# Performance work log

Hardware: AMD Instinct MI355X
Metric: run time of the kernel (lower is better)

## Reference

```python
import jax, jax.numpy as jnp
import numpy as np

B, C, H, W = 32, 64, 32, 32
DIM = H * W          # number of tokens (pixels)
DEPTH = 8
TAU = 1.0
NUM_CLASSES = 10


def setup_inputs() -> dict:
    key = jax.random.key(0)
    ks = jax.random.split(key, 6)
    return {
        "image": jax.random.normal(ks[0], (B, C, H, W), dtype=jnp.float32),
        "WV": 10.0 * jax.random.normal(ks[1], (C, C), dtype=jnp.float32),
        "WK": jax.random.normal(ks[2], (C, C), dtype=jnp.float32),
        "WQ": jax.random.normal(ks[3], (C, C), dtype=jnp.float32),
        "last_W": jax.random.normal(ks[4], (NUM_CLASSES, DIM), dtype=jnp.float32) / np.sqrt(DIM),
        "last_b": jnp.zeros((NUM_CLASSES,), dtype=jnp.float32),
    }


def reference(image, WV, WK, WQ, last_W, last_b):
    # flatten(2).transpose(1,2): (B,C,H,W) -> (B, H*W, C)
    X = image.reshape(B, C, DIM).transpose(0, 2, 1)
    scale = DIM ** (-0.5)
    for _ in range(DEPTH):
        # weight_sharing=True, sign=0 -> W = WV every layer
        Q = X @ WQ                                  # (B, n, C)
        K = X @ WK                                  # (B, n, C)
        scores = jnp.einsum('bnc,bmc->bnm', Q, K) * scale  # (B, n, n)
        A = jax.nn.softmax(scores, axis=-1)
        # diffusion_step (method 'A'): tau * A @ (X @ W) + X
        X = TAU * jnp.einsum('bnm,bmc->bnc', A, X @ WV) + X
    # mean over channel dim -> (B, dim), then Linear(dim, num_classes)
    pred = X.mean(-1) @ last_W.T + last_b
    return pred
```

## Files before the change

### kernel.cpp

```cpp
#include <hip/hip_runtime.h>
#include <math.h>

#define BB    32
#define CCH   64
#define DIMN  1024
#define NCLS  10

typedef __attribute__((ext_vector_type(8))) short bf16x8;
typedef __attribute__((ext_vector_type(4))) float f32x4;
typedef __attribute__((ext_vector_type(4))) unsigned short us4;
typedef __attribute__((ext_vector_type(8))) unsigned short us8;

#define MFMA16(a, b, c) __builtin_amdgcn_mfma_f32_16x16x32_bf16(a, b, c, 0, 0, 0)

__device__ __forceinline__ unsigned short f2bf(float x) {
  unsigned u = __float_as_uint(x);
  unsigned r = u + 0x7fffu + ((u >> 16) & 1u);
  return (unsigned short)(r >> 16);
}
__device__ __forceinline__ float bf2f(unsigned short h) {
  return __uint_as_float(((unsigned)h) << 16);
}
__device__ __forceinline__ void split3_pk(float x0, float x1,
                                          unsigned& hp, unsigned& mp,
                                          unsigned& lp) {
  unsigned h, m, l;
  asm("v_cvt_pk_bf16_f32 %0, %1, %2" : "=v"(h) : "v"(x0), "v"(x1));
  const float h0 = __uint_as_float(h << 16);
  const float h1 = __uint_as_float(h & 0xffff0000u);
  const float r0 = x0 - h0, r1 = x1 - h1;
  asm("v_cvt_pk_bf16_f32 %0, %1, %2" : "=v"(m) : "v"(r0), "v"(r1));
  const float m0 = __uint_as_float(m << 16);
  const float m1 = __uint_as_float(m & 0xffff0000u);
  asm("v_cvt_pk_bf16_f32 %0, %1, %2" : "=v"(l) : "v"(r0 - m0), "v"(r1 - m1));
  hp = h; mp = m; lp = l;
}
__device__ __forceinline__ void split3_pk2(float x0, float x1,
    unsigned short& h0, unsigned short& m0, unsigned short& l0,
    unsigned short& h1, unsigned short& m1, unsigned short& l1) {
  unsigned h, m, l;
  split3_pk(x0, x1, h, m, l);
  h0 = (unsigned short)h; h1 = (unsigned short)(h >> 16);
  m0 = (unsigned short)m; m1 = (unsigned short)(m >> 16);
  l0 = (unsigned short)l; l1 = (unsigned short)(l >> 16);
}
__device__ __forceinline__ void split3_frag(const float* xv, bf16x8& fh,
                                            bf16x8& fm, bf16x8& fl) {
  union U { bf16x8 v; unsigned d[4]; } uh, um, ul;
  #pragma unroll
  for (int p = 0; p < 4; ++p)
    split3_pk(xv[2 * p], xv[2 * p + 1], uh.d[p], um.d[p], ul.d[p]);
  fh = uh.v; fm = um.v; fl = ul.v;
}
__device__ __forceinline__ bf16x8 ld16B(const unsigned short* p) {
  union { us8 u; bf16x8 v; } c;
  c.u = *(const us8*)p;
  return c.v;
}

__global__ __launch_bounds__(256) void k_transpose(const float* __restrict__ img,
                                                   float* __restrict__ X) {
  __shared__ float tile[64][65];
  const int b  = blockIdx.y;
  const int n0 = blockIdx.x * 64;
  const int tx = threadIdx.x & 63;
  const int ty = threadIdx.x >> 6;
  const float* src = img + (size_t)b * CCH * DIMN;
  #pragma unroll
  for (int c = ty; c < 64; c += 4)
    tile[c][tx] = src[(size_t)c * DIMN + n0 + tx];
  __syncthreads();
  float* dst = X + (size_t)b * DIMN * CCH;
  #pragma unroll
  for (int nn = ty; nn < 64; nn += 4)
    dst[(size_t)(n0 + nn) * CCH + tx] = tile[tx][nn];
}

__global__ __launch_bounds__(256) void k_qkv_split(
    const float* __restrict__ X,
    const float* __restrict__ WQ, const float* __restrict__ WK,
    const float* __restrict__ WV,
    float* __restrict__ Q,
    unsigned short* __restrict__ Kh, unsigned short* __restrict__ Km,
    unsigned short* __restrict__ Kl,
    unsigned short* __restrict__ VhT, unsigned short* __restrict__ VmT,
    unsigned short* __restrict__ VlT) {
  __shared__ float xs[16][64];
  __shared__ unsigned short vs[3][16][64];
  const int c  = threadIdx.x & 63;
  const int tg = threadIdx.x >> 6;
  const size_t t0 = (size_t)blockIdx.x * 16;
  #pragma unroll
  for (int r = tg; r < 16; r += 4)
    xs[r][c] = X[(t0 + r) * 64 + c];
  __syncthreads();
  float qa[4] = {0.f,0.f,0.f,0.f};
  float ka[4] = {0.f,0.f,0.f,0.f};
  float va[4] = {0.f,0.f,0.f,0.f};
  for (int j = 0; j < 64; ++j) {
    const float wq = WQ[j * 64 + c];
    const float wk = WK[j * 64 + c];
    const float wv = WV[j * 64 + c];
    #pragma unroll
    for (int r = 0; r < 4; ++r) {
      const float x = xs[tg * 4 + r][j];
      qa[r] = fmaf(x, wq, qa[r]);
      ka[r] = fmaf(x, wk, ka[r]);
      va[r] = fmaf(x, wv, va[r]);
    }
  }
  #pragma unroll
  for (int pr = 0; pr < 2; ++pr) {
    const int r0 = 2 * pr, r1 = 2 * pr + 1;
    const int ta = tg * 4 + r0, tb = tg * 4 + r1;
    const size_t ia = (t0 + ta) * 64 + c;
    const size_t ib = (t0 + tb) * 64 + c;
    Q[ia] = qa[r0]; Q[ib] = qa[r1];
    unsigned short h0, m0, l0, h1, m1, l1;
    split3_pk2(ka[r0], ka[r1], h0, m0, l0, h1, m1, l1);
    Kh[ia] = h0; Km[ia] = m0; Kl[ia] = l0;
    Kh[ib] = h1; Km[ib] = m1; Kl[ib] = l1;
    split3_pk2(va[r0], va[r1], h0, m0, l0, h1, m1, l1);
    vs[0][ta][c] = h0; vs[1][ta][c] = m0; vs[2][ta][c] = l0;
    vs[0][tb][c] = h1; vs[1][tb][c] = m1; vs[2][tb][c] = l1;
  }
  __syncthreads();
  {
    const int row  = threadIdx.x >> 2;
    const int part = threadIdx.x & 3;
    const size_t bofs = (t0 >> 10) * ((size_t)DIMN * 64);
    const size_t kt   = (t0 & 1023) >> 5;
    const size_t tin  = (size_t)part * 8 + ((t0 & 31) >> 2);
    unsigned short* dst[3] = {VhT, VmT, VlT};
    #pragma unroll
    for (int term = 0; term < 3; ++term) {
      us4 pk;
      #pragma unroll
      for (int i = 0; i < 4; ++i) pk[i] = vs[term][part * 4 + i][row];
      *(us4*)&dst[term][bofs + kt * 2048 + (size_t)row * 32 + tin] = pk;
    }
  }
}

__global__ __launch_bounds__(256) void k_qkv_merge(
    float* __restrict__ X,
    const float* __restrict__ Mp, const float* __restrict__ Lp,
    const float* __restrict__ Op,
    const float* __restrict__ WQ, const float* __restrict__ WK,
    const float* __restrict__ WV,
    float* __restrict__ Q,
    unsigned short* __restrict__ Kh, unsigned short* __restrict__ Km,
    unsigned short* __restrict__ Kl,
    unsigned short* __restrict__ VhT, unsigned short* __restrict__ VmT,
    unsigned short* __restrict__ VlT) {
  __shared__ float xs[16][64];
  __shared__ unsigned short vs[3][16][64];
  const int c  = threadIdx.x & 63;
  const int tg = threadIdx.x >> 6;
  const size_t t0 = (size_t)blockIdx.x * 16;
  #pragma unroll
  for (int r = tg; r < 16; r += 4) {
    const size_t grow = t0 + r;
    const float m0 = Mp[grow], m1 = Mp[32768 + grow];
    const float l0 = Lp[grow], l1 = Lp[32768 + grow];
    const float mm = fmaxf(m0, m1);
    const float w0 = __expf(m0 - mm), w1 = __expf(m1 - mm);
    const float inv = 1.0f / (l0 * w0 + l1 * w1);
    const float o0 = Op[grow * 64 + c];
    const float o1 = Op[(size_t)2097152 + grow * 64 + c];
    const float xn = X[grow * 64 + c] + (o0 * w0 + o1 * w1) * inv;
    X[grow * 64 + c] = xn;
    xs[r][c] = xn;
  }
  __syncthreads();
  float qa[4] = {0.f,0.f,0.f,0.f};
  float ka[4] = {0.f,0.f,0.f,0.f};
  float va[4] = {0.f,0.f,0.f,0.f};
  for (int j = 0; j < 64; ++j) {
    const float wq = WQ[j * 64 + c];
    const float wk = WK[j * 64 + c];
    const float wv = WV[j * 64 + c];
    #pragma unroll
    for (int r = 0; r < 4; ++r) {
      const float x = xs[tg * 4 + r][j];
      qa[r] = fmaf(x, wq, qa[r]);
      ka[r] = fmaf(x, wk, ka[r]);
      va[r] = fmaf(x, wv, va[r]);
    }
  }
  #pragma unroll
  for (int pr = 0; pr < 2; ++pr) {
    const int r0 = 2 * pr, r1 = 2 * pr + 1;
    const int ta = tg * 4 + r0, tb = tg * 4 + r1;
    const size_t ia = (t0 + ta) * 64 + c;
    const size_t ib = (t0 + tb) * 64 + c;
    Q[ia] = qa[r0]; Q[ib] = qa[r1];
    unsigned short h0, m0, l0, h1, m1, l1;
    split3_pk2(ka[r0], ka[r1], h0, m0, l0, h1, m1, l1);
    Kh[ia] = h0; Km[ia] = m0; Kl[ia] = l0;
    Kh[ib] = h1; Km[ib] = m1; Kl[ib] = l1;
    split3_pk2(va[r0], va[r1], h0, m0, l0, h1, m1, l1);
    vs[0][ta][c] = h0; vs[1][ta][c] = m0; vs[2][ta][c] = l0;
    vs[0][tb][c] = h1; vs[1][tb][c] = m1; vs[2][tb][c] = l1;
  }
  __syncthreads();
  {
    const int row  = threadIdx.x >> 2;
    const int part = threadIdx.x & 3;
    const size_t bofs = (t0 >> 10) * ((size_t)DIMN * 64);
    const size_t kt   = (t0 & 1023) >> 5;
    const size_t tin  = (size_t)part * 8 + ((t0 & 31) >> 2);
    unsigned short* dst[3] = {VhT, VmT, VlT};
    #pragma unroll
    for (int term = 0; term < 3; ++term) {
      us4 pk;
      #pragma unroll
      for (int i = 0; i < 4; ++i) pk[i] = vs[term][part * 4 + i][row];
      *(us4*)&dst[term][bofs + kt * 2048 + (size_t)row * 32 + tin] = pk;
    }
  }
}

__global__ __launch_bounds__(256, 4) void k_attn_sk(
    const float* __restrict__ Qg,
    const unsigned short* __restrict__ Kh, const unsigned short* __restrict__ Km,
    const unsigned short* __restrict__ Kl,
    const unsigned short* __restrict__ VhT, const unsigned short* __restrict__ VmT,
    const unsigned short* __restrict__ VlT,
    float* __restrict__ Mp, float* __restrict__ Lp, float* __restrict__ Op) {
  __shared__ __align__(16) unsigned short Khs[32 * 72];
  __shared__ __align__(16) unsigned short Kms[32 * 72];
  __shared__ __align__(16) unsigned short Kls[32 * 72];
  __shared__ __align__(16) unsigned short Vhs[64 * 40];
  __shared__ __align__(16) unsigned short Vms[64 * 40];
  __shared__ __align__(16) unsigned short Vls[64 * 40];

  const int tid  = threadIdx.x;
  const int w    = tid >> 6;
  const int lane = tid & 63;
  const int ln   = lane & 15;
  const int q    = lane >> 4;

  const int bid   = blockIdx.x;
  const int xcd   = bid & 7;
  const int seq   = bid >> 3;
  const int b     = xcd * 4 + (seq >> 5);
  const int local = seq & 31;
  const int half  = local >> 4;
  const int i0    = (local & 15) * 64;

  const size_t base = (size_t)b * (DIMN * 64);
  const float scale = 0.03125f;

  const int kj = tid >> 3, kg = tid & 7;
  const int vc = tid >> 2, vg = tid & 3;
  const int klo = kj * 72 + kg * 8;
  const int vlo = vc * 40 + vg * 8;

  bf16x8 qh[2], qm[2], ql[2];
  {
    const int mrow = i0 + 16 * w + ln;
    const float* qp = Qg + base + (size_t)mrow * 64 + 8 * q;
    #pragma unroll
    for (int s = 0; s < 2; ++s) {
      const float4 x0 = ((const float4*)(qp + 32 * s))[0];
      const float4 x1 = ((const float4*)(qp + 32 * s))[1];
      const float xv[8] = {x0.x, x0.y, x0.z, x0.w, x1.x, x1.y, x1.z, x1.w};
      split3_frag(xv, qh[s], qm[s], ql[s]);
    }
  }

  f32x4 O[4];
  #pragma unroll
  for (int ct = 0; ct < 4; ++ct) O[ct] = (f32x4){0.f, 0.f, 0.f, 0.f};
  float m_run = -INFINITY;
  float l_run = 0.f;

  const int kt0 = half * 16;
  for (int kt = kt0; kt < kt0 + 16; ++kt) {
    __syncthreads();

    {
      const size_t tof = base + (size_t)kt * 2048 + tid * 8;
      const us8 a0 = *(const us8*)&Kh[tof];
      const us8 a1 = *(const us8*)&Km[tof];
      const us8 a2 = *(const us8*)&Kl[tof];
      const us8 b0 = *(const us8*)&VhT[tof];
      const us8 b1 = *(const us8*)&VmT[tof];
      const us8 b2 = *(const us8*)&VlT[tof];
      *(us8*)&Khs[klo] = a0;
      *(us8*)&Kms[klo] = a1;
      *(us8*)&Kls[klo] = a2;
      *(us8*)&Vhs[vlo] = b0;
      *(us8*)&Vms[vlo] = b1;
      *(us8*)&Vls[vlo] = b2;
    }
    __syncthreads();

    f32x4 sacc[2];
    __builtin_amdgcn_s_setprio(1);
    #pragma unroll
    for (int ct = 0; ct < 2; ++ct) {
      f32x4 a = (f32x4){0.f, 0.f, 0.f, 0.f};
      #pragma unroll
      for (int s = 0; s < 2; ++s) {
        const int ko = (16 * ct + ln) * 72 + 32 * s + 8 * q;
        const bf16x8 bh = ld16B(&Khs[ko]);
        const bf16x8 bm = ld16B(&Kms[ko]);
        const bf16x8 bl = ld16B(&Kls[ko]);
        a = MFMA16(bh, ql[s], a);
        a = MFMA16(bl, qh[s], a);
        a = MFMA16(bm, qm[s], a);
        a = MFMA16(bh, qm[s], a);
        a = MFMA16(bm, qh[s], a);
        a = MFMA16(bh, qh[s], a);
      }
      sacc[ct] = a;
    }
    __builtin_amdgcn_s_setprio(0);

    float m8 = fmaxf(fmaxf(fmaxf(sacc[0][0], sacc[0][1]),
                           fmaxf(sacc[0][2], sacc[0][3])),
                     fmaxf(fmaxf(sacc[1][0], sacc[1][1]),
                           fmaxf(sacc[1][2], sacc[1][3])));
    m8 = fmaxf(m8, __shfl_xor(m8, 16, 64));
    m8 = fmaxf(m8, __shfl_xor(m8, 32, 64));
    const float mnew  = fmaxf(m_run, m8 * scale);
    const float alpha = __expf(m_run - mnew);
    m_run = mnew;

    float pv[8];
    float s8 = 0.f;
    #pragma unroll
    for (int ct = 0; ct < 2; ++ct) {
      #pragma unroll
      for (int r = 0; r < 4; ++r) {
        const float p = __expf(sacc[ct][r] * scale - m_run);
        pv[ct * 4 + r] = p;
        s8 += p;
      }
    }
    float sr = s8 + __shfl_xor(s8, 16, 64);
    sr = sr + __shfl_xor(sr, 32, 64);
    l_run = l_run * alpha + sr;

    const int srcb = (lane & 48) + ((lane & 48) >> 2);
    float arow[4];
    #pragma unroll
    for (int r = 0; r < 4; ++r) arow[r] = __shfl(alpha, srcb + r, 64);
    #pragma unroll
    for (int ct = 0; ct < 4; ++ct) {
      #pragma unroll
      for (int r = 0; r < 4; ++r) O[ct][r] *= arow[r];
    }

    bf16x8 ph, pm, pl;
    split3_frag(pv, ph, pm, pl);

    __builtin_amdgcn_s_setprio(1);
    #pragma unroll
    for (int ct = 0; ct < 4; ++ct) {
      const int vo = (16 * ct + ln) * 40 + 8 * q;
      const bf16x8 vvh = ld16B(&Vhs[vo]);
      const bf16x8 vvm = ld16B(&Vms[vo]);
      const bf16x8 vvl = ld16B(&Vls[vo]);
      O[ct] = MFMA16(ph, vvh, O[ct]);
      O[ct] = MFMA16(ph, vvm, O[ct]);
      O[ct] = MFMA16(pm, vvh, O[ct]);
      O[ct] = MFMA16(pm, vvm, O[ct]);
      O[ct] = MFMA16(ph, vvl, O[ct]);
      O[ct] = MFMA16(pl, vvh, O[ct]);
    }
    __builtin_amdgcn_s_setprio(0);
  }

  const size_t hofs = (size_t)half * (32 * 1024);
  #pragma unroll
  for (int r = 0; r < 4; ++r) {
    const int row = i0 + 16 * w + 4 * q + r;
    const size_t grow = hofs + (size_t)b * DIMN + row;
    #pragma unroll
    for (int ct = 0; ct < 4; ++ct)
      Op[grow * 64 + ln + 16 * ct] = O[ct][r];
  }
  if (q == 0) {
    const size_t tgrow = hofs + (size_t)b * DIMN + i0 + 16 * w + ln;
    Mp[tgrow] = m_run;
    Lp[tgrow] = l_run;
  }
}

__global__ __launch_bounds__(256) void k_merge_mean(
    const float* __restrict__ X,
    const float* __restrict__ Mp, const float* __restrict__ Lp,
    const float* __restrict__ Op, float* __restrict__ meanv) {
  const int c  = threadIdx.x & 63;
  const int tg = threadIdx.x >> 6;
  const size_t t0 = (size_t)blockIdx.x * 128;
  for (int i = tg; i < 128; i += 4) {
    const size_t grow = t0 + i;
    const float m0 = Mp[grow], m1 = Mp[32768 + grow];
    const float l0 = Lp[grow], l1 = Lp[32768 + grow];
    const float mm = fmaxf(m0, m1);
    const float w0 = __expf(m0 - mm), w1 = __expf(m1 - mm);
    const float inv = 1.0f / (l0 * w0 + l1 * w1);
    const float o0 = Op[grow * 64 + c];
    const float o1 = Op[(size_t)2097152 + grow * 64 + c];
    float v = X[grow * 64 + c] + (o0 * w0 + o1 * w1) * inv;
    #pragma unroll
    for (int off = 32; off > 0; off >>= 1)
      v += __shfl_down(v, off, 64);
    if (c == 0) meanv[grow] = v * (1.0f / 64.0f);
  }
}

__global__ __launch_bounds__(256) void k_head2(
    const float* __restrict__ meanv, const float* __restrict__ lW,
    const float* __restrict__ lb, float* __restrict__ out) {
  __shared__ float red[256];
  const int b   = blockIdx.x;
  const int tid = threadIdx.x;
  float acc[NCLS];
  #pragma unroll
  for (int k = 0; k < NCLS; ++k) acc[k] = 0.f;
  for (int n = tid; n < DIMN; n += 256) {
    const float m = meanv[(size_t)b * DIMN + n];
    #pragma unroll
    for (int k = 0; k < NCLS; ++k)
      acc[k] = fmaf(m, lW[k * DIMN + n], acc[k]);
  }
  for (int k = 0; k < NCLS; ++k) {
    red[tid] = acc[k];
    __syncthreads();
    for (int s = 128; s > 0; s >>= 1) {
      if (tid < s) red[tid] += red[tid + s];
      __syncthreads();
    }
    if (tid == 0) out[b * NCLS + k] = red[0] + lb[k];
    __syncthreads();
  }
}

__global__ __launch_bounds__(256) void k_attn_s(
    const float* __restrict__ Qg,
    const unsigned short* __restrict__ Kh, const unsigned short* __restrict__ Km,
    const unsigned short* __restrict__ Kl,
    const unsigned short* __restrict__ VhT, const unsigned short* __restrict__ VmT,
    const unsigned short* __restrict__ VlT,
    float* __restrict__ X, float* __restrict__ meanout) {
  __shared__ __align__(16) unsigned short Khs[32 * 72];
  __shared__ __align__(16) unsigned short Kms[32 * 72];
  __shared__ __align__(16) unsigned short Kls[32 * 72];
  __shared__ __align__(16) unsigned short Vhs[64 * 40];
  __shared__ __align__(16) unsigned short Vms[64 * 40];
  __shared__ __align__(16) unsigned short Vls[64 * 40];

  const int tid  = threadIdx.x;
  const int w    = tid >> 6;
  const int lane = tid & 63;
  const int ln   = lane & 15;
  const int q    = lane >> 4;
  const int bid = blockIdx.x;
  const int xcd = bid & 7;
  const int seq = bid >> 3;
  const int b   = xcd * 4 + (seq >> 4);
  const int i0  = (seq & 15) * 64;
  const size_t base = (size_t)b * (DIMN * 64);
  const float scale = 0.03125f;

  const int kj = tid >> 3, kg = tid & 7;
  const int vc = tid >> 2, vg = tid & 3;
  const int klo = kj * 72 + kg * 8;
  const int vlo = vc * 40 + vg * 8;

  bf16x8 qh[2], qm[2], ql[2];
  {
    const int mrow = i0 + 16 * w + ln;
    const float* qp = Qg + base + (size_t)mrow * 64 + 8 * q;
    #pragma unroll
    for (int s = 0; s < 2; ++s) {
      const float4 x0 = ((const float4*)(qp + 32 * s))[0];
      const float4 x1 = ((const float4*)(qp + 32 * s))[1];
      const float xv[8] = {x0.x, x0.y, x0.z, x0.w, x1.x, x1.y, x1.z, x1.w};
      split3_frag(xv, qh[s], qm[s], ql[s]);
    }
  }

  f32x4 O[4];
  #pragma unroll
  for (int ct = 0; ct < 4; ++ct) O[ct] = (f32x4){0.f, 0.f, 0.f, 0.f};
  float m_run = -INFINITY;
  float l_run = 0.f;

  for (int kt = 0; kt < 32; ++kt) {
    __syncthreads();
    {
      const size_t tof = base + (size_t)kt * 2048 + tid * 8;
      const us8 a0 = *(const us8*)&Kh[tof];
      const us8 a1 = *(const us8*)&Km[tof];
      const us8 a2 = *(const us8*)&Kl[tof];
      const us8 b0 = *(const us8*)&VhT[tof];
      const us8 b1 = *(const us8*)&VmT[tof];
      const us8 b2 = *(const us8*)&VlT[tof];
      *(us8*)&Khs[klo] = a0;
      *(us8*)&Kms[klo] = a1;
      *(us8*)&Kls[klo] = a2;
      *(us8*)&Vhs[vlo] = b0;
      *(us8*)&Vms[vlo] = b1;
      *(us8*)&Vls[vlo] = b2;
    }
    __syncthreads();

    f32x4 sacc[2];
    __builtin_amdgcn_s_setprio(1);
    #pragma unroll
    for (int ct = 0; ct < 2; ++ct) {
      f32x4 a = (f32x4){0.f, 0.f, 0.f, 0.f};
      #pragma unroll
      for (int s = 0; s < 2; ++s) {
        const int ko = (16 * ct + ln) * 72 + 32 * s + 8 * q;
        const bf16x8 bh = ld16B(&Khs[ko]);
        const bf16x8 bm = ld16B(&Kms[ko]);
        const bf16x8 bl = ld16B(&Kls[ko]);
        a = MFMA16(bh, ql[s], a);
        a = MFMA16(bl, qh[s], a);
        a = MFMA16(bm, qm[s], a);
        a = MFMA16(bh, qm[s], a);
        a = MFMA16(bm, qh[s], a);
        a = MFMA16(bh, qh[s], a);
      }
      sacc[ct] = a;
    }
    __builtin_amdgcn_s_setprio(0);

    float m8 = fmaxf(fmaxf(fmaxf(sacc[0][0], sacc[0][1]),
                           fmaxf(sacc[0][2], sacc[0][3])),
                     fmaxf(fmaxf(sacc[1][0], sacc[1][1]),
                           fmaxf(sacc[1][2], sacc[1][3])));
    m8 = fmaxf(m8, __shfl_xor(m8, 16, 64));
    m8 = fmaxf(m8, __shfl_xor(m8, 32, 64));
    const float mnew  = fmaxf(m_run, m8 * scale);
    const float alpha = __expf(m_run - mnew);
    m_run = mnew;

    float pv[8];
    float s8 = 0.f;
    #pragma unroll
    for (int ct = 0; ct < 2; ++ct) {
      #pragma unroll
      for (int r = 0; r < 4; ++r) {
        const float p = __expf(sacc[ct][r] * scale - m_run);
        pv[ct * 4 + r] = p;
        s8 += p;
      }
    }
    float sr = s8 + __shfl_xor(s8, 16, 64);
    sr = sr + __shfl_xor(sr, 32, 64);
    l_run = l_run * alpha + sr;

    const int srcb = (lane & 48) + ((lane & 48) >> 2);
    float arow[4];
    #pragma unroll
    for (int r = 0; r < 4; ++r) arow[r] = __shfl(alpha, srcb + r, 64);
    #pragma unroll
    for (int ct = 0; ct < 4; ++ct) {
      #pragma unroll
      for (int r = 0; r < 4; ++r) O[ct][r] *= arow[r];
    }

    bf16x8 ph, pm, pl;
    split3_frag(pv, ph, pm, pl);

    __builtin_amdgcn_s_setprio(1);
    #pragma unroll
    for (int ct = 0; ct < 4; ++ct) {
      const int vo = (16 * ct + ln) * 40 + 8 * q;
      const bf16x8 vvh = ld16B(&Vhs[vo]);
      const bf16x8 vvm = ld16B(&Vms[vo]);
      const bf16x8 vvl = ld16B(&Vls[vo]);
      O[ct] = MFMA16(ph, vvh, O[ct]);
      O[ct] = MFMA16(ph, vvm, O[ct]);
      O[ct] = MFMA16(pm, vvh, O[ct]);
      O[ct] = MFMA16(pm, vvm, O[ct]);
      O[ct] = MFMA16(ph, vvl, O[ct]);
      O[ct] = MFMA16(pl, vvh, O[ct]);
    }
    __builtin_amdgcn_s_setprio(0);
  }

  const int srcb = (lane & 48) + ((lane & 48) >> 2);
  float linv[4];
  #pragma unroll
  for (int r = 0; r < 4; ++r) linv[r] = 1.0f / __shfl(l_run, srcb + r, 64);
  #pragma unroll
  for (int r = 0; r < 4; ++r) {
    const int row = i0 + 16 * w + 4 * q + r;
    float srow = 0.f;
    #pragma unroll
    for (int ct = 0; ct < 4; ++ct) {
      float* xp = X + base + (size_t)row * 64 + ln + 16 * ct;
      const float nv = *xp + O[ct][r] * linv[r];
      *xp = nv;
      srow += nv;
    }
    if (meanout) {
      #pragma unroll
      for (int mk = 1; mk <= 8; mk <<= 1)
        srow += __shfl_xor(srow, mk, 64);
      if (ln == 0) meanout[(size_t)b * DIMN + row] = srow * (1.0f / 64.0f);
    }
  }
}

extern "C" void kernel_launch(void* const* d_in, const int* in_sizes, int n_in,
                              void* d_out, int out_size, void* d_ws, size_t ws_size,
                              hipStream_t stream) {
  const float* image = (const float*)d_in[0];
  const float* WV    = (const float*)d_in[1];
  const float* WK    = (const float*)d_in[2];
  const float* WQ    = (const float*)d_in[3];
  const float* lW    = (const float*)d_in[4];
  const float* lb    = (const float*)d_in[5];
  float* out = (float*)d_out;

  float* ws = (float*)d_ws;
  const size_t NELEM = (size_t)BB * DIMN * CCH;
  const size_t NROW  = (size_t)BB * DIMN;

  const size_t need_sk   = (7 * NELEM + 5 * NROW) * sizeof(float);
  const size_t need_fast = (5 * NELEM + NROW) * sizeof(float);

  if (ws_size >= need_sk) {
    float* X = ws;
    float* Q = ws + NELEM;
    unsigned short* Kh  = (unsigned short*)(ws + 2 * NELEM);
    unsigned short* Km  = Kh + NELEM;
    unsigned short* Kl  = Kh + 2 * NELEM;
    unsigned short* VhT = Kh + 3 * NELEM;
    unsigned short* VmT = Kh + 4 * NELEM;
    unsigned short* VlT = Kh + 5 * NELEM;
    float* Op    = ws + 5 * NELEM;
    float* Mp    = ws + 7 * NELEM;
    float* Lp    = Mp + 2 * NROW;
    float* meanv = Lp + 2 * NROW;

    k_transpose<<<dim3(DIMN / 64, BB), 256, 0, stream>>>(image, X);
    k_qkv_split<<<(BB * DIMN) / 16, 256, 0, stream>>>(
        X, WQ, WK, WV, Q, Kh, Km, Kl, VhT, VmT, VlT);
    for (int layer = 0; layer < 8; ++layer) {
      k_attn_sk<<<1024, 256, 0, stream>>>(
          Q, Kh, Km, Kl, VhT, VmT, VlT, Mp, Lp, Op);
      if (layer < 7)
        k_qkv_merge<<<(BB * DIMN) / 16, 256, 0, stream>>>(
            X, Mp, Lp, Op, WQ, WK, WV, Q, Kh, Km, Kl, VhT, VmT, VlT);
    }
    k_merge_mean<<<256, 256, 0, stream>>>(X, Mp, Lp, Op, meanv);
    k_head2<<<BB, 256, 0, stream>>>(meanv, lW, lb, out);
  } else {
    float* X = ws;
    float* Q = ws + NELEM;
    unsigned short* Kh  = (unsigned short*)(ws + 2 * NELEM);
    unsigned short* Km  = Kh + NELEM;
    unsigned short* Kl  = Kh + 2 * NELEM;
    unsigned short* VhT = Kh + 3 * NELEM;
    unsigned short* VmT = Kh + 4 * NELEM;
    unsigned short* VlT = Kh + 5 * NELEM;
    float* meanv = ws + 5 * NELEM;
    (void)need_fast;

    k_transpose<<<dim3(DIMN / 64, BB), 256, 0, stream>>>(image, X);
    for (int layer = 0; layer < 8; ++layer) {
      k_qkv_split<<<(BB * DIMN) / 16, 256, 0, stream>>>(
          X, WQ, WK, WV, Q, Kh, Km, Kl, VhT, VmT, VlT);
      k_attn_s<<<512, 256, 0, stream>>>(
          Q, Kh, Km, Kl, VhT, VmT, VlT, X, (layer == 7) ? meanv : nullptr);
    }
    k_head2<<<BB, 256, 0, stream>>>(meanv, lW, lb, out);
  }
}
```

Baseline: 717.7 us.

## Process two query tiles per attention block to reuse staged K/V

Each attention workgroup now handles 128 query rows (two 64-row tiles) instead of 64, so each K/V tile staged into shared memory feeds twice the MFMA work. The grid is halved and launch bounds drop to 2 waves-per-SIMD occupancy to allow the doubled accumulators and Q fragments in registers. The QKV projection inner loop is also rewritten to read x from shared memory as float4 vectors, and setprio hints are dropped from the fallback attention kernel. The trade-off is fewer resident blocks and higher register pressure, which reduces latency hiding.

```diff
diff --git a/kernel.cpp b/kernel.cpp
--- a/kernel.cpp
+++ b/kernel.cpp
@@ -74,6 +74,32 @@
   #pragma unroll
   for (int nn = ty; nn < 64; nn += 4)
     dst[(size_t)(n0 + nn) * CCH + tx] = tile[tx][nn];
+}
+
+__device__ __forceinline__ void qkv_inner(
+    const float xs[16][64],
+    const float* __restrict__ WQ, const float* __restrict__ WK,
+    const float* __restrict__ WV, int c, int tg,
+    float qa[4], float ka[4], float va[4]) {
+  for (int j = 0; j < 64; j += 4) {
+    float4 xv[4];
+    #pragma unroll
+    for (int r = 0; r < 4; ++r)
+      xv[r] = *(const float4*)&xs[tg * 4 + r][j];
+    #pragma unroll
+    for (int jj = 0; jj < 4; ++jj) {
+      const float wq = WQ[(j + jj) * 64 + c];
+      const float wk = WK[(j + jj) * 64 + c];
+      const float wv = WV[(j + jj) * 64 + c];
+      #pragma unroll
+      for (int r = 0; r < 4; ++r) {
+        const float x = ((const float*)&xv[r])[jj];
+        qa[r] = fmaf(x, wq, qa[r]);
+        ka[r] = fmaf(x, wk, ka[r]);
+        va[r] = fmaf(x, wv, va[r]);
+      }
+    }
+  }
 }
 
 __global__ __launch_bounds__(256) void k_qkv_split(
@@ -97,18 +123,7 @@
   float qa[4] = {0.f,0.f,0.f,0.f};
   float ka[4] = {0.f,0.f,0.f,0.f};
   float va[4] = {0.f,0.f,0.f,0.f};
-  for (int j = 0; j < 64; ++j) {
-    const float wq = WQ[j * 64 + c];
-    const float wk = WK[j * 64 + c];
-    const float wv = WV[j * 64 + c];
-    #pragma unroll
-    for (int r = 0; r < 4; ++r) {
-      const float x = xs[tg * 4 + r][j];
-      qa[r] = fmaf(x, wq, qa[r]);
-      ka[r] = fmaf(x, wk, ka[r]);
-      va[r] = fmaf(x, wv, va[r]);
-    }
-  }
+  qkv_inner(xs, WQ, WK, WV, c, tg, qa, ka, va);
   #pragma unroll
   for (int pr = 0; pr < 2; ++pr) {
     const int r0 = 2 * pr, r1 = 2 * pr + 1;
@@ -176,18 +191,7 @@
   float qa[4] = {0.f,0.f,0.f,0.f};
   float ka[4] = {0.f,0.f,0.f,0.f};
   float va[4] = {0.f,0.f,0.f,0.f};
-  for (int j = 0; j < 64; ++j) {
-    const float wq = WQ[j * 64 + c];
-    const float wk = WK[j * 64 + c];
-    const float wv = WV[j * 64 + c];
-    #pragma unroll
-    for (int r = 0; r < 4; ++r) {
-      const float x = xs[tg * 4 + r][j];
-      qa[r] = fmaf(x, wq, qa[r]);
-      ka[r] = fmaf(x, wk, ka[r]);
-      va[r] = fmaf(x, wv, va[r]);
-    }
-  }
+  qkv_inner(xs, WQ, WK, WV, c, tg, qa, ka, va);
   #pragma unroll
   for (int pr = 0; pr < 2; ++pr) {
     const int r0 = 2 * pr, r1 = 2 * pr + 1;
@@ -221,7 +225,7 @@
   }
 }
 
-__global__ __launch_bounds__(256, 4) void k_attn_sk(
+__global__ __launch_bounds__(256, 2) void k_attn_sk(
     const float* __restrict__ Qg,
     const unsigned short* __restrict__ Kh, const unsigned short* __restrict__ Km,
     const unsigned short* __restrict__ Kl,
@@ -244,10 +248,10 @@
   const int bid   = blockIdx.x;
   const int xcd   = bid & 7;
   const int seq   = bid >> 3;
-  const int b     = xcd * 4 + (seq >> 5);
-  const int local = seq & 31;
-  const int half  = local >> 4;
-  const int i0    = (local & 15) * 64;
+  const int b     = xcd * 4 + (seq >> 4);
+  const int local = seq & 15;
+  const int half  = local >> 3;
+  const int i0    = (local & 7) * 128;
 
   const size_t base = (size_t)b * (DIMN * 64);
   const float scale = 0.03125f;
@@ -257,24 +261,27 @@
   const int klo = kj * 72 + kg * 8;
   const int vlo = vc * 40 + vg * 8;
 
-  bf16x8 qh[2], qm[2], ql[2];
-  {
-    const int mrow = i0 + 16 * w + ln;
+  bf16x8 qh[2][2], qm[2][2], ql[2][2];
+  #pragma unroll
+  for (int t = 0; t < 2; ++t) {
+    const int mrow = i0 + 64 * t + 16 * w + ln;
     const float* qp = Qg + base + (size_t)mrow * 64 + 8 * q;
     #pragma unroll
     for (int s = 0; s < 2; ++s) {
       const float4 x0 = ((const float4*)(qp + 32 * s))[0];
       const float4 x1 = ((const float4*)(qp + 32 * s))[1];
       const float xv[8] = {x0.x, x0.y, x0.z, x0.w, x1.x, x1.y, x1.z, x1.w};
-      split3_frag(xv, qh[s], qm[s], ql[s]);
-    }
-  }
-
-  f32x4 O[4];
-  #pragma unroll
-  for (int ct = 0; ct < 4; ++ct) O[ct] = (f32x4){0.f, 0.f, 0.f, 0.f};
-  float m_run = -INFINITY;
-  float l_run = 0.f;
+      split3_frag(xv, qh[t][s], qm[t][s], ql[t][s]);
+    }
+  }
+
+  f32x4 O[2][4];
+  #pragma unroll
+  for (int t = 0; t < 2; ++t)
+    #pragma unroll
+    for (int ct = 0; ct < 4; ++ct) O[t][ct] = (f32x4){0.f, 0.f, 0.f, 0.f};
+  float m_run[2] = {-INFINITY, -INFINITY};
+  float l_run[2] = {0.f, 0.f};
 
   const int kt0 = half * 16;
   for (int kt = kt0; kt < kt0 + 16; ++kt) {
@@ -297,65 +304,75 @@
     }
     __syncthreads();
 
-    f32x4 sacc[2];
+    f32x4 sacc[2][2];
     __builtin_amdgcn_s_setprio(1);
     #pragma unroll
     for (int ct = 0; ct < 2; ++ct) {
-      f32x4 a = (f32x4){0.f, 0.f, 0.f, 0.f};
+      f32x4 aA = (f32x4){0.f, 0.f, 0.f, 0.f};
+      f32x4 aB = (f32x4){0.f, 0.f, 0.f, 0.f};
       #pragma unroll
       for (int s = 0; s < 2; ++s) {
         const int ko = (16 * ct + ln) * 72 + 32 * s + 8 * q;
         const bf16x8 bh = ld16B(&Khs[ko]);
         const bf16x8 bm = ld16B(&Kms[ko]);
         const bf16x8 bl = ld16B(&Kls[ko]);
-        a = MFMA16(bh, ql[s], a);
-        a = MFMA16(bl, qh[s], a);
-        a = MFMA16(bm, qm[s], a);
-        a = MFMA16(bh, qm[s], a);
-        a = MFMA16(bm, qh[s], a);
-        a = MFMA16(bh, qh[s], a);
+        aA = MFMA16(bh, ql[0][s], aA);
+        aA = MFMA16(bl, qh[0][s], aA);
+        aA = MFMA16(bm, qm[0][s], aA);
+        aA = MFMA16(bh, qm[0][s], aA);
+        aA = MFMA16(bm, qh[0][s], aA);
+        aA = MFMA16(bh, qh[0][s], aA);
+        aB = MFMA16(bh, ql[1][s], aB);
+        aB = MFMA16(bl, qh[1][s], aB);
+        aB = MFMA16(bm, qm[1][s], aB);
+        aB = MFMA16(bh, qm[1][s], aB);
+        aB = MFMA16(bm, qh[1][s], aB);
+        aB = MFMA16(bh, qh[1][s], aB);
       }
-      sacc[ct] = a;
+      sacc[0][ct] = aA; sacc[1][ct] = aB;
     }
     __builtin_amdgcn_s_setprio(0);
 
-    float m8 = fmaxf(fmaxf(fmaxf(sacc[0][0], sacc[0][1]),
-                           fmaxf(sacc[0][2], sacc[0][3])),
-                     fmaxf(fmaxf(sacc[1][0], sacc[1][1]),
-                           fmaxf(sacc[1][2], sacc[1][3])));
-    m8 = fmaxf(m8, __shfl_xor(m8, 16, 64));
-    m8 = fmaxf(m8, __shfl_xor(m8, 32, 64));
-    const float mnew  = fmaxf(m_run, m8 * scale);
-    const float alpha = __expf(m_run - mnew);
-    m_run = mnew;
-
-    float pv[8];
-    float s8 = 0.f;
-    #pragma unroll
-    for (int ct = 0; ct < 2; ++ct) {
-      #pragma unroll
-      for (int r = 0; r < 4; ++r) {
-        const float p = __expf(sacc[ct][r] * scale - m_run);
-        pv[ct * 4 + r] = p;
-        s8 += p;
+    bf16x8 ph[2], pm[2], pl[2];
+    const int srcb = (lane & 48) + ((lane & 48) >> 2);
+    #pragma unroll
+    for (int t = 0; t < 2; ++t) {
+      float m8 = fmaxf(fmaxf(fmaxf(sacc[t][0][0], sacc[t][0][1]),
+                             fmaxf(sacc[t][0][2], sacc[t][0][3])),
+                       fmaxf(fmaxf(sacc[t][1][0], sacc[t][1][1]),
+                             fmaxf(sacc[t][1][2], sacc[t][1][3])));
+      m8 = fmaxf(m8, __shfl_xor(m8, 16, 64));
+      m8 = fmaxf(m8, __shfl_xor(m8, 32, 64));
+      const float mnew  = fmaxf(m_run[t], m8 * scale);
+      const float alpha = __expf(m_run[t] - mnew);
+      m_run[t] = mnew;
+
+      float pv[8];
+      float s8 = 0.f;
+      #pragma unroll
+      for (int ct = 0; ct < 2; ++ct) {
+        #pragma unroll
+        for (int r = 0; r < 4; ++r) {
+          const float p = __expf(sacc[t][ct][r] * scale - m_run[t]);
+          pv[ct * 4 + r] = p;
+          s8 += p;
+        }
       }
-    }
-    float sr = s8 + __shfl_xor(s8, 16, 64);
-    sr = sr + __shfl_xor(sr, 32, 64);
-    l_run = l_run * alpha + sr;
-
-    const int srcb = (lane & 48) + ((lane & 48) >> 2);
-    float arow[4];
-    #pragma unroll
-    for (int r = 0; r < 4; ++r) arow[r] = __shfl(alpha, srcb + r, 64);
-    #pragma unroll
-    for (int ct = 0; ct < 4; ++ct) {
-      #pragma unroll
-      for (int r = 0; r < 4; ++r) O[ct][r] *= arow[r];
-    }
-
-    bf16x8 ph, pm, pl;
-    split3_frag(pv, ph, pm, pl);
+      float sr = s8 + __shfl_xor(s8, 16, 64);
+      sr = sr + __shfl_xor(sr, 32, 64);
+      l_run[t] = l_run[t] * alpha + sr;
+
+      float arow[4];
+      #pragma unroll
+      for (int r = 0; r < 4; ++r) arow[r] = __shfl(alpha, srcb + r, 64);
+      #pragma unroll
+      for (int ct = 0; ct < 4; ++ct) {
+        #pragma unroll
+        for (int r = 0; r < 4; ++r) O[t][ct][r] *= arow[r];
+      }
+
+      split3_frag(pv, ph[t], pm[t], pl[t]);
+    }
 
     __builtin_amdgcn_s_setprio(1);
     #pragma unroll
@@ -364,29 +381,39 @@
       const bf16x8 vvh = ld16B(&Vhs[vo]);
       const bf16x8 vvm = ld16B(&Vms[vo]);
       const bf16x8 vvl = ld16B(&Vls[vo]);
-      O[ct] = MFMA16(ph, vvh, O[ct]);
-      O[ct] = MFMA16(ph, vvm, O[ct]);
-      O[ct] = MFMA16(pm, vvh, O[ct]);
-      O[ct] = MFMA16(pm, vvm, O[ct]);
-      O[ct] = MFMA16(ph, vvl, O[ct]);
-      O[ct] = MFMA16(pl, vvh, O[ct]);
+      O[0][ct] = MFMA16(ph[0], vvh, O[0][ct]);
+      O[0][ct] = MFMA16(ph[0], vvm, O[0][ct]);
+      O[0][ct] = MFMA16(pm[0], vvh, O[0][ct]);
+      O[0][ct] = MFMA16(pm[0], vvm, O[0][ct]);
+      O[0][ct] = MFMA16(ph[0], vvl, O[0][ct]);
+      O[0][ct] = MFMA16(pl[0], vvh, O[0][ct]);
+      O[1][ct] = MFMA16(ph[1], vvh, O[1][ct]);
+      O[1][ct] = MFMA16(ph[1], vvm, O[1][ct]);
+      O[1][ct] = MFMA16(pm[1], vvh, O[1][ct]);
+      O[1][ct] = MFMA16(pm[1], vvm, O[1][ct]);
+      O[1][ct] = MFMA16(ph[1], vvl, O[1][ct]);
+      O[1][ct] = MFMA16(pl[1], vvh, O[1][ct]);
     }
     __builtin_amdgcn_s_setprio(0);
   }
 
   const size_t hofs = (size_t)half * (32 * 1024);
   #pragma unroll
-  for (int r = 0; r < 4; ++r) {
-    const int row = i0 + 16 * w + 4 * q + r;
-    const size_t grow = hofs + (size_t)b * DIMN + row;
-    #pragma unroll
-    for (int ct = 0; ct < 4; ++ct)
-      Op[grow * 64 + ln + 16 * ct] = O[ct][r];
-  }
-  if (q == 0) {
-    const size_t tgrow = hofs + (size_t)b * DIMN + i0 + 16 * w + ln;
-    Mp[tgrow] = m_run;
-    Lp[tgrow] = l_run;
+  for (int t = 0; t < 2; ++t) {
+    const int ti0 = i0 + 64 * t;
+    #pragma unroll
+    for (int r = 0; r < 4; ++r) {
+      const int row = ti0 + 16 * w + 4 * q + r;
+      const size_t grow = hofs + (size_t)b * DIMN + row;
+      #pragma unroll
+      for (int ct = 0; ct < 4; ++ct)
+        Op[grow * 64 + ln + 16 * ct] = O[t][ct][r];
+    }
+    if (q == 0) {
+      const size_t tgrow = hofs + (size_t)b * DIMN + ti0 + 16 * w + ln;
+      Mp[tgrow] = m_run[t];
+      Lp[tgrow] = l_run[t];
+    }
   }
 }
 
@@ -512,7 +539,6 @@
     __syncthreads();
 
     f32x4 sacc[2];
-    __builtin_amdgcn_s_setprio(1);
     #pragma unroll
     for (int ct = 0; ct < 2; ++ct) {
       f32x4 a = (f32x4){0.f, 0.f, 0.f, 0.f};
@@ -531,7 +557,6 @@
       }
       sacc[ct] = a;
     }
-    __builtin_amdgcn_s_setprio(0);
 
     float m8 = fmaxf(fmaxf(fmaxf(sacc[0][0], sacc[0][1]),
                            fmaxf(sacc[0][2], sacc[0][3])),
@@ -571,7 +596,6 @@
     bf16x8 ph, pm, pl;
     split3_frag(pv, ph, pm, pl);
 
-    __builtin_amdgcn_s_setprio(1);
     #pragma unroll
     for (int ct = 0; ct < 4; ++ct) {
       const int vo = (16 * ct + ln) * 40 + 8 * q;
@@ -585,7 +609,6 @@
       O[ct] = MFMA16(ph, vvl, O[ct]);
       O[ct] = MFMA16(pl, vvh, O[ct]);
     }
-    __builtin_amdgcn_s_setprio(0);
   }
 
   const int srcb = (lane & 48) + ((lane & 48) >> 2);
@@ -648,7 +671,7 @@
     k_qkv_split<<<(BB * DIMN) / 16, 256, 0, stream>>>(
         X, WQ, WK, WV, Q, Kh, Km, Kl, VhT, VmT, VlT);
     for (int layer = 0; layer < 8; ++layer) {
-      k_attn_sk<<<1024, 256, 0, stream>>>(
+      k_attn_sk<<<512, 256, 0, stream>>>(
           Q, Kh, Km, Kl, VhT, VmT, VlT, Mp, Lp, Op);
       if (layer < 7)
         k_qkv_merge<<<(BB * DIMN) / 16, 256, 0, stream>>>(
```

Result: faster. 700.9 us (-2.3%).
